# Kernel tuning notes

Hardware: AMD Instinct MI355X
Metric: run time of the kernel (lower is better)

## Reference

```python
import jax, jax.numpy as jnp
import numpy as np

DIM = 64; PDIM = 16; HEADS = 8; WS = 10; KS = 13; NBLK = 2
B = 4; H = 200; W = 200


def conv2d(x, w, b=None, padding=0, groups=1):
    out = jax.lax.conv_general_dilated(
        x, w, (1, 1), [(padding, padding), (padding, padding)],
        dimension_numbers=('NCHW', 'OIHW', 'NCHW'), feature_group_count=groups)
    if b is not None:
        out = out + b[None, :, None, None]
    return out


def gelu(x):
    return jax.nn.gelu(x, approximate=False)  # torch default exact gelu


def layernorm_cf(x, w, b, eps=1e-6):
    # channels_first LayerNorm: normalize over channel axis (axis=1)
    mu = jnp.mean(x, axis=1, keepdims=True)
    var = jnp.mean((x - mu) ** 2, axis=1, keepdims=True)
    return (x - mu) * jax.lax.rsqrt(var + eps) * w[None, :, None, None] + b[None, :, None, None]


def conv_ffn(x, pw, pb, dw, db, aw, ab):
    x = gelu(conv2d(x, pw, pb))
    x = gelu(conv2d(x, dw, db, padding=dw.shape[-1] // 2, groups=x.shape[1])) + x
    return conv2d(x, aw, ab)


def geo_ensemble(k):
    k = jax.lax.stop_gradient(k)  # torch code uses .detach()
    kr = jnp.rot90(k, k=-1, axes=(2, 3))
    s = k + k[:, :, :, ::-1] + k[:, :, ::-1, :] + k[:, :, ::-1, ::-1]
    s = s + kr + kr[:, :, :, ::-1] + kr[:, :, ::-1, :] + kr[:, :, ::-1, ::-1]
    return s / 8.0


def rpe_bias(rpb, ws):
    idx = jnp.arange(ws * ws)
    h_, w_ = idx // ws, idx % ws
    rel_h = h_[None, :] - h_[:, None] + ws - 1  # k_h - q_h
    rel_w = w_[None, :] - w_[:, None] + ws - 1
    rel_idx = rel_h * (2 * ws - 1) + rel_w
    return rpb[:, rel_idx]  # [heads, N, N]


def window_attention(x, qw, qb, ow, ob, rpb):
    b, c, h, w = x.shape  # h, w divisible by WS
    hd, wd = h // WS, w // WS
    ch = c // HEADS
    qkv = conv2d(x, qw, qb)  # [b, 3c, h, w]
    t = qkv.reshape(b, 3, HEADS, ch, hd, WS, wd, WS)
    t = t.transpose(1, 0, 4, 6, 2, 5, 7, 3).reshape(3, b * hd * wd, HEADS, WS * WS, ch)
    q, k, v = t[0], t[1], t[2]
    bias = rpe_bias(rpb, WS)[None]  # [1, heads, N, N]
    score = jnp.einsum('whqc,whkc->whqk', q, k) / jnp.sqrt(jnp.float32(ch)) + bias
    attn = jax.nn.softmax(score, axis=-1)
    out = jnp.einsum('whqk,whkc->whqc', attn, v)
    out = out.reshape(b, hd, wd, HEADS, WS, WS, ch).transpose(0, 3, 6, 1, 4, 2, 5).reshape(b, c, h, w)
    return conv2d(out, ow, ob)


def conv_attention(x, lk, d1w, d1b, d2w, d2b):
    bs, c, h, w = x.shape
    x1, x2 = x[:, :PDIM], x[:, PDIM:]
    g = jnp.mean(x1, axis=(2, 3), keepdims=True)  # AdaptiveAvgPool2d(1)
    g = gelu(conv2d(g, d1w, d1b))
    dk = conv2d(g, d2w, d2b).reshape(bs * PDIM, 1, 3, 3)  # per-sample dw kernels
    x1d = conv2d(x1.reshape(1, bs * PDIM, h, w), dk, padding=1, groups=bs * PDIM)
    x1d = x1d.reshape(bs, PDIM, h, w)
    x1 = conv2d(x1, lk, padding=KS // 2) + x1d
    return jnp.concatenate([x1, x2], axis=1)


def _forward(x, ln_proj_w, ln_proj_b, proj_p_w, proj_p_b, proj_d_w, proj_d_b, proj_a_w, proj_a_b,
             ln_attn_w, ln_attn_b, qkv_w, qkv_b, attn_out_w, attn_out_b, rpb,
             dwcp1_w, dwcp1_b, dwcp2_w, dwcp2_b, pconv_aggr_w, pconv_aggr_b,
             ffn_p_w, ffn_p_b, ffn_d_w, ffn_d_b, ffn_a_w, ffn_a_b,
             ln_out_w, ln_out_b, conv_out_w, conv_out_b, plk_filter):
    skip = x
    x = layernorm_cf(x, ln_proj_w, ln_proj_b)
    x = conv_ffn(x, proj_p_w, proj_p_b, proj_d_w, proj_d_b, proj_a_w, proj_a_b)
    x = x + window_attention(layernorm_cf(x, ln_attn_w, ln_attn_b), qkv_w, qkv_b, attn_out_w, attn_out_b, rpb)
    lk = geo_ensemble(plk_filter)
    for i in range(NBLK):  # lns are Identity (use_ln=False)
        y = conv_ffn(x, ffn_p_w[i], ffn_p_b[i], ffn_d_w[i], ffn_d_b[i], ffn_a_w[i], ffn_a_b[i])
        y = conv_attention(y, lk, dwcp1_w[i], dwcp1_b[i], dwcp2_w[i], dwcp2_b[i])
        y = conv2d(y, pconv_aggr_w[i], pconv_aggr_b[i])
        x = x + y
    x = conv2d(layernorm_cf(x, ln_out_w, ln_out_b), conv_out_w, conv_out_b, padding=1)
    return x + skip


def setup_inputs() -> dict:
    key = jax.random.key(0)
    ks = jax.random.split(key, 20)
    def rn(i, shape, scale):
        return jax.random.normal(ks[i], shape, dtype=jnp.float32) * scale
    inp = {
        'x': rn(0, (B, DIM, H, W), 1.0),
        'ln_proj_w': jnp.ones(DIM, jnp.float32), 'ln_proj_b': jnp.zeros(DIM, jnp.float32),
        'proj_p_w': rn(1, (128, 64, 1, 1), 64 ** -0.5), 'proj_p_b': jnp.zeros(128, jnp.float32),
        'proj_d_w': rn(2, (128, 1, 3, 3), 1.0 / 3.0), 'proj_d_b': jnp.zeros(128, jnp.float32),
        'proj_a_w': rn(3, (64, 128, 1, 1), 128 ** -0.5), 'proj_a_b': jnp.zeros(64, jnp.float32),
        'ln_attn_w': jnp.ones(DIM, jnp.float32), 'ln_attn_b': jnp.zeros(DIM, jnp.float32),
        'qkv_w': rn(4, (192, 64, 1, 1), 64 ** -0.5), 'qkv_b': jnp.zeros(192, jnp.float32),
        'attn_out_w': rn(5, (64, 64, 1, 1), 64 ** -0.5), 'attn_out_b': jnp.zeros(64, jnp.float32),
        'rpb': rn(6, (HEADS, (2 * WS - 1) ** 2), 0.001),
        'dwcp1_w': rn(7, (2, 8, 16, 1, 1), 16 ** -0.5), 'dwcp1_b': jnp.zeros((2, 8), jnp.float32),
        'dwcp2_w': rn(8, (2, 144, 8, 1, 1), 0.01), 'dwcp2_b': jnp.zeros((2, 144), jnp.float32),
        'pconv_aggr_w': rn(9, (2, 64, 64, 1, 1), 64 ** -0.5), 'pconv_aggr_b': jnp.zeros((2, 64), jnp.float32),
        'ffn_p_w': rn(10, (2, 80, 64, 1, 1), 64 ** -0.5), 'ffn_p_b': jnp.zeros((2, 80), jnp.float32),
        'ffn_d_w': rn(11, (2, 80, 1, 3, 3), 1.0 / 3.0), 'ffn_d_b': jnp.zeros((2, 80), jnp.float32),
        'ffn_a_w': rn(12, (2, 64, 80, 1, 1), 80 ** -0.5), 'ffn_a_b': jnp.zeros((2, 64), jnp.float32),
        'ln_out_w': jnp.ones(DIM, jnp.float32), 'ln_out_b': jnp.zeros(DIM, jnp.float32),
        'conv_out_w': rn(13, (64, 64, 3, 3), (64 * 9) ** -0.5), 'conv_out_b': jnp.zeros(64, jnp.float32),
        'plk_filter': rn(14, (PDIM, PDIM, KS, KS), (PDIM * KS * KS) ** -0.5),
    }
    return inp


def reference(x, ln_proj_w, ln_proj_b, proj_p_w, proj_p_b, proj_d_w, proj_d_b, proj_a_w, proj_a_b,
              ln_attn_w, ln_attn_b, qkv_w, qkv_b, attn_out_w, attn_out_b, rpb,
              dwcp1_w, dwcp1_b, dwcp2_w, dwcp2_b, pconv_aggr_w, pconv_aggr_b,
              ffn_p_w, ffn_p_b, ffn_d_w, ffn_d_b, ffn_a_w, ffn_a_b,
              ln_out_w, ln_out_b, conv_out_w, conv_out_b, plk_filter):
    return _forward(x, ln_proj_w, ln_proj_b, proj_p_w, proj_p_b, proj_d_w, proj_d_b, proj_a_w, proj_a_b,
                    ln_attn_w, ln_attn_b, qkv_w, qkv_b, attn_out_w, attn_out_b, rpb,
                    dwcp1_w, dwcp1_b, dwcp2_w, dwcp2_b, pconv_aggr_w, pconv_aggr_b,
                    ffn_p_w, ffn_p_b, ffn_d_w, ffn_d_b, ffn_a_w, ffn_a_b,
                    ln_out_w, ln_out_b, conv_out_w, conv_out_b, plk_filter)
```

## Files before the change

kernel.cpp:

```cpp
#include <hip/hip_runtime.h>
#include <math.h>

#define HH 200
#define WW 200
#define HWP 40000
#define NP4 10000
#define BB 4

#define LKS 40
#define DPS 24
#define PARTSZ 2560000

typedef __fp16 f16x2 __attribute__((ext_vector_type(2)));
typedef __fp16 f16x8 __attribute__((ext_vector_type(8)));
typedef float fx4 __attribute__((ext_vector_type(4)));

#if __has_builtin(__builtin_amdgcn_fdot2)
__device__ __forceinline__ float fdot2f(f16x2 a, f16x2 b, float c) {
    return __builtin_amdgcn_fdot2(a, b, c, false);
}
#else
__device__ __forceinline__ float fdot2f(f16x2 a, f16x2 b, float c) {
    return c + (float)a[0] * (float)b[0] + (float)a[1] * (float)b[1];
}
#endif

__device__ __forceinline__ f16x2 pk2(float a, float b) {
    return __builtin_amdgcn_cvt_pkrtz(a, b);
}

__device__ __forceinline__ float gelu_f(float x) {
    return 0.5f * x * (1.0f + erff(x * 0.7071067811865475f));
}

__global__ __launch_bounds__(256) void prep_kernel(
    const float* __restrict__ pc, f16x2* __restrict__ wth)
{
    int i = blockIdx.x * 256 + threadIdx.x;
    if (i >= 4096) return;
    int w = i >> 11;
    int r = i & 2047;
    int c2 = r / 64, o = r - c2 * 64;
    const float* src = pc + w * 4096;
    f16x2 v;
    v[0] = (__fp16)src[o * 64 + 2 * c2];
    v[1] = (__fp16)src[o * 64 + 2 * c2 + 1];
    wth[w * 2048 + r] = v;
}

__global__ __launch_bounds__(256) void prepA_kernel(
    const float* __restrict__ qkvw, const float* __restrict__ pp,
    const float* __restrict__ ao, const float* __restrict__ fp,
    f16x8* __restrict__ wA)
{
    int s = blockIdx.x * 256 + threadIdx.x;
    if (s >= 4352) return;
    const float* src;
    int base;
    if (s < 1536)      { src = qkvw;      base = 0; }
    else if (s < 2560) { src = pp;        base = 1536; }
    else if (s < 3072) { src = ao;        base = 2560; }
    else if (s < 3712) { src = fp;        base = 3072; }
    else               { src = fp + 5120; base = 3712; }
    int r = s - base;
    int lane = r & 63;
    int t = r >> 6;
    int ks = t & 1;
    int cot = t >> 1;
    int co = cot * 16 + (lane & 15);
    int k0 = ks * 32 + ((lane >> 4) << 3);
    f16x8 v;
#pragma unroll
    for (int j = 0; j < 8; ++j) v[j] = (__fp16)src[co * 64 + k0 + j];
    wA[s] = v;
}

__global__ __launch_bounds__(256) void prepA2_kernel(
    const float* __restrict__ pa, const float* __restrict__ fa,
    f16x8* __restrict__ wA2)
{
    int s = blockIdx.x * 256 + threadIdx.x;
    if (s >= 2560) return;
    const float* src; int base, Ci, ksteps;
    if (s < 1024)      { src = pa;        base = 0;    Ci = 128; ksteps = 4; }
    else if (s < 1792) { src = fa;        base = 1024; Ci = 80;  ksteps = 3; }
    else               { src = fa + 5120; base = 1792; Ci = 80;  ksteps = 3; }
    int r = s - base;
    int lane = r & 63;
    int u = r >> 6;
    int ks = u % ksteps;
    int cot = u / ksteps;
    int co = cot * 16 + (lane & 15);
    int k0 = ks * 32 + ((lane >> 4) << 3);
    f16x8 v;
#pragma unroll
    for (int j = 0; j < 8; ++j) {
        int k = k0 + j;
        v[j] = (k < Ci) ? (__fp16)src[co * Ci + k] : (__fp16)0.f;
    }
    wA2[s] = v;
}

__global__ __launch_bounds__(256) void prepA3_kernel(
    const float* __restrict__ co3, f16x8* __restrict__ wA3)
{
    int s = blockIdx.x * 256 + threadIdx.x;
    if (s >= 4608) return;
    int lane = s & 63;
    int u = s >> 6;
    int cot = u & 3;
    int t = u >> 2;
    int co = cot * 16 + (lane & 15);
    int k0 = t * 32 + ((lane >> 4) << 3);
    f16x8 v;
#pragma unroll
    for (int j = 0; j < 8; ++j) {
        int k = k0 + j;
        int tap = k >> 6, ci = k & 63;
        v[j] = (__fp16)co3[(co * 64 + ci) * 9 + tap];
    }
    wA3[s] = v;
}

__global__ __launch_bounds__(256, 2) void ln_kernel(
    const float* __restrict__ in, const float* __restrict__ w,
    const float* __restrict__ b, __fp16* __restrict__ out)
{
    int p = blockIdx.x * 256 + threadIdx.x;
    int bb = blockIdx.y;
    if (p >= HWP) return;
    const float* ib = in + (size_t)bb * 64 * HWP + p;
    float v[64];
    float mu = 0.f;
#pragma unroll
    for (int c = 0; c < 64; ++c) { v[c] = ib[(size_t)c * HWP]; mu += v[c]; }
    mu *= (1.f / 64.f);
    float var = 0.f;
#pragma unroll
    for (int c = 0; c < 64; ++c) { float d = v[c] - mu; var += d * d; }
    var *= (1.f / 64.f);
    float r = rsqrtf(var + 1e-6f);
    __fp16* ob = out + (size_t)bb * 64 * HWP + p;
#pragma unroll
    for (int c = 0; c < 64; ++c) ob[(size_t)c * HWP] = (__fp16)((v[c] - mu) * r * w[c] + b[c]);
}

__global__ __launch_bounds__(256, 2) void lnconvh_kernel(
    const float* __restrict__ in,
    const float* __restrict__ lnw, const float* __restrict__ lnb,
    const f16x8* __restrict__ wA,
    const float* __restrict__ bias, __fp16* __restrict__ outh,
    int Co, int do_gelu)
{
    int lane = threadIdx.x & 63;
    int wv = threadIdx.x >> 6;
    int px0 = blockIdx.x * 256 + wv * 64;
    if (px0 >= HWP) return;
    int bb = blockIdx.z;
    int cot0 = blockIdx.y * 4;
    int nCot = (Co >> 4) - cot0; if (nCot > 4) nCot = 4;
    int row = lane >> 4;
    int colp = lane & 15;

    float wl[2][8], bl[2][8];
#pragma unroll
    for (int ks = 0; ks < 2; ++ks)
#pragma unroll
        for (int j = 0; j < 8; ++j) {
            int c = ks * 32 + row * 8 + j;
            wl[ks][j] = lnw[c];
            bl[ks][j] = lnb[c];
        }

    f16x8 afr[4][2];
#pragma unroll
    for (int c = 0; c < 4; ++c)
        if (c < nCot)
#pragma unroll
            for (int ks = 0; ks < 2; ++ks)
                afr[c][ks] = wA[(((cot0 + c) * 2 + ks) << 6) + lane];

    fx4 acc[4][4];
#pragma unroll
    for (int c = 0; c < 4; ++c)
#pragma unroll
        for (int nt = 0; nt < 4; ++nt)
#pragma unroll
            for (int r = 0; r < 4; ++r) acc[c][nt][r] = 0.f;

    const float* ib = in + (size_t)bb * 64 * HWP;
#pragma unroll
    for (int nt = 0; nt < 4; ++nt) {
        int px = px0 + nt * 16 + colp;
        float xv[2][8];
        float s = 0.f, sq = 0.f;
#pragma unroll
        for (int ks = 0; ks < 2; ++ks)
#pragma unroll
            for (int j = 0; j < 8; ++j) {
                float v = ib[(size_t)(ks * 32 + row * 8 + j) * HWP + px];
                xv[ks][j] = v;
                s += v; sq += v * v;
            }
        s += __shfl_xor(s, 16, 64);  sq += __shfl_xor(sq, 16, 64);
        s += __shfl_xor(s, 32, 64);  sq += __shfl_xor(sq, 32, 64);
        float mu = s * (1.f / 64.f);
        float var = sq * (1.f / 64.f) - mu * mu;
        float rr = rsqrtf(fmaxf(var, 0.f) + 1e-6f);
#pragma unroll
        for (int ks = 0; ks < 2; ++ks) {
            union { f16x8 v; f16x2 h[4]; } bu;
#pragma unroll
            for (int j2 = 0; j2 < 4; ++j2) {
                float v0 = (xv[ks][2 * j2]     - mu) * rr * wl[ks][2 * j2]     + bl[ks][2 * j2];
                float v1 = (xv[ks][2 * j2 + 1] - mu) * rr * wl[ks][2 * j2 + 1] + bl[ks][2 * j2 + 1];
                bu.h[j2] = pk2(v0, v1);
            }
#pragma unroll
            for (int c = 0; c < 4; ++c)
                if (c < nCot)
                    acc[c][nt] = __builtin_amdgcn_mfma_f32_16x16x32_f16(afr[c][ks], bu.v, acc[c][nt], 0, 0, 0);
        }
    }

#pragma unroll
    for (int c = 0; c < 4; ++c) {
        if (c < nCot) {
#pragma unroll
            for (int r = 0; r < 4; ++r) {
                int co = (cot0 + c) * 16 + row * 4 + r;
                float bv = bias[co];
#pragma unroll
                for (int nt = 0; nt < 4; ++nt) {
                    int px = px0 + nt * 16 + colp;
                    float v = acc[c][nt][r] + bv;
                    if (do_gelu) v = gelu_f(v);
                    outh[((size_t)bb * Co + co) * HWP + px] = (__fp16)v;
                }
            }
        }
    }
}

__global__ __launch_bounds__(256, 2) void conv1x1_mfma_kernel(
    const float* __restrict__ in, const f16x8* __restrict__ wA,
    const float* __restrict__ bias, float* outf, __fp16* outh,
    int Co, int do_gelu, int do_add)
{
    int lane = threadIdx.x & 63;
    int wv = threadIdx.x >> 6;
    int px0 = blockIdx.x * 256 + wv * 64;
    if (px0 >= HWP) return;
    int bb = blockIdx.z;
    int cot0 = blockIdx.y * 4;
    int nCot = (Co >> 4) - cot0; if (nCot > 4) nCot = 4;
    int row = lane >> 4;
    int colp = lane & 15;

    fx4 acc[4][4];
#pragma unroll
    for (int c = 0; c < 4; ++c)
#pragma unroll
        for (int nt = 0; nt < 4; ++nt)
#pragma unroll
            for (int r = 0; r < 4; ++r) acc[c][nt][r] = 0.f;

    const float* ib = in + (size_t)bb * 64 * HWP;
#pragma unroll
    for (int ks = 0; ks < 2; ++ks) {
        f16x8 afr[4];
#pragma unroll
        for (int c = 0; c < 4; ++c)
            if (c < nCot) afr[c] = wA[(((cot0 + c) * 2 + ks) << 6) + lane];
#pragma unroll
        for (int nt = 0; nt < 4; ++nt) {
            int px = px0 + nt * 16 + colp;
            const float* bp = ib + (size_t)(ks * 32 + row * 8) * HWP + px;
            union { f16x8 v; f16x2 h[4]; } bu;
            bu.h[0] = pk2(bp[0],              bp[(size_t)1 * HWP]);
            bu.h[1] = pk2(bp[(size_t)2 * HWP], bp[(size_t)3 * HWP]);
            bu.h[2] = pk2(bp[(size_t)4 * HWP], bp[(size_t)5 * HWP]);
            bu.h[3] = pk2(bp[(size_t)6 * HWP], bp[(size_t)7 * HWP]);
#pragma unroll
            for (int c = 0; c < 4; ++c)
                if (c < nCot)
                    acc[c][nt] = __builtin_amdgcn_mfma_f32_16x16x32_f16(afr[c], bu.v, acc[c][nt], 0, 0, 0);
        }
    }

#pragma unroll
    for (int c = 0; c < 4; ++c) {
        if (c < nCot) {
#pragma unroll
            for (int r = 0; r < 4; ++r) {
                int co = (cot0 + c) * 16 + row * 4 + r;
                float bv = bias[co];
#pragma unroll
                for (int nt = 0; nt < 4; ++nt) {
                    int px = px0 + nt * 16 + colp;
                    float v = acc[c][nt][r] + bv;
                    if (do_gelu) v = gelu_f(v);
                    if (outh) {
                        outh[((size_t)bb * Co + co) * HWP + px] = (__fp16)v;
                    } else {
                        float* op = outf + ((size_t)bb * Co + co) * HWP;
                        if (do_add) v += op[px];
                        op[px] = v;
                    }
                }
            }
        }
    }
}

__global__ __launch_bounds__(256, 2) void convh_kernel(
    const __fp16* __restrict__ in,
    const f16x8* __restrict__ wA,
    const float* __restrict__ bias, float* outf, __fp16* outh,
    int Ci, int ksteps, int Co, int do_gelu, int do_add)
{
    int lane = threadIdx.x & 63;
    int wv = threadIdx.x >> 6;
    int px0 = blockIdx.x * 256 + wv * 64;
    if (px0 >= HWP) return;
    int bb = blockIdx.z;
    int cot0 = blockIdx.y * 4;
    int nCot = (Co >> 4) - cot0; if (nCot > 4) nCot = 4;
    int row = lane >> 4;
    int colp = lane & 15;

    fx4 acc[4][4];
#pragma unroll
    for (int c = 0; c < 4; ++c)
#pragma unroll
        for (int nt = 0; nt < 4; ++nt)
#pragma unroll
            for (int r = 0; r < 4; ++r) acc[c][nt][r] = 0.f;

    const __fp16* ib = in + (size_t)bb * Ci * HWP;
    for (int ks = 0; ks < ksteps; ++ks) {
        f16x8 afr[4];
#pragma unroll
        for (int c = 0; c < 4; ++c)
            if (c < nCot) afr[c] = wA[(((cot0 + c) * ksteps + ks) << 6) + lane];
        int k0 = ks * 32 + row * 8;
        bool ok = (k0 < Ci);
#pragma unroll
        for (int nt = 0; nt < 4; ++nt) {
            int px = px0 + nt * 16 + colp;
            f16x8 bv;
            if (ok) {
                const __fp16* bp = ib + (size_t)k0 * HWP + px;
#pragma unroll
                for (int j = 0; j < 8; ++j) bv[j] = bp[(size_t)j * HWP];
            } else {
#pragma unroll
                for (int j = 0; j < 8; ++j) bv[j] = (__fp16)0.f;
            }
#pragma unroll
            for (int c = 0; c < 4; ++c)
                if (c < nCot)
                    acc[c][nt] = __builtin_amdgcn_mfma_f32_16x16x32_f16(afr[c], bv, acc[c][nt], 0, 0, 0);
        }
    }

#pragma unroll
    for (int c = 0; c < 4; ++c) {
        if (c < nCot) {
#pragma unroll
            for (int r = 0; r < 4; ++r) {
                int co = (cot0 + c) * 16 + row * 4 + r;
                float bv = bias[co];
#pragma unroll
                for (int nt = 0; nt < 4; ++nt) {
                    int px = px0 + nt * 16 + colp;
                    float v = acc[c][nt][r] + bv;
                    if (do_gelu) v = gelu_f(v);
                    if (outh) {
                        outh[((size_t)bb * Co + co) * HWP + px] = (__fp16)v;
                    } else {
                        float* op = outf + ((size_t)bb * Co + co) * HWP;
                        if (do_add) v += op[px];
                        op[px] = v;
                    }
                }
            }
        }
    }
}

__global__ __launch_bounds__(256, 2) void conv3_mfma_kernel(
    const __fp16* __restrict__ in,
    const f16x8* __restrict__ wA3,
    const float* __restrict__ bias, const float* __restrict__ skip,
    float* __restrict__ out)
{
    int lane = threadIdx.x & 63;
    int wv = threadIdx.x >> 6;
    int px0 = blockIdx.x * 256 + wv * 64;
    if (px0 >= HWP) return;
    int bb = blockIdx.z;
    int row = lane >> 4;
    int colp = lane & 15;

    fx4 acc[4][4];
#pragma unroll
    for (int c = 0; c < 4; ++c)
#pragma unroll
        for (int nt = 0; nt < 4; ++nt)
#pragma unroll
            for (int r = 0; r < 4; ++r) acc[c][nt][r] = 0.f;

    int py[4], pxx[4];
#pragma unroll
    for (int nt = 0; nt < 4; ++nt) {
        int p = px0 + nt * 16 + colp;
        py[nt] = p / WW;
        pxx[nt] = p - py[nt] * WW;
    }

    const __fp16* ib = in + (size_t)bb * 64 * HWP;
    for (int t = 0; t < 18; ++t) {
        int tap = t >> 1, ks = t & 1;
        int dy = tap / 3 - 1, dx = tap % 3 - 1;
        f16x8 afr[4];
#pragma unroll
        for (int c = 0; c < 4; ++c) afr[c] = wA3[((t * 4 + c) << 6) + lane];
        const __fp16* kb = ib + (size_t)(ks * 32 + row * 8) * HWP;
#pragma unroll
        for (int nt = 0; nt < 4; ++nt) {
            int yy = py[nt] + dy, xx = pxx[nt] + dx;
            f16x8 bv;
            if ((unsigned)yy < HH && (unsigned)xx < WW) {
                const __fp16* bp = kb + yy * WW + xx;
#pragma unroll
                for (int j = 0; j < 8; ++j) bv[j] = bp[(size_t)j * HWP];
            } else {
#pragma unroll
                for (int j = 0; j < 8; ++j) bv[j] = (__fp16)0.f;
            }
#pragma unroll
            for (int c = 0; c < 4; ++c)
                acc[c][nt] = __builtin_amdgcn_mfma_f32_16x16x32_f16(afr[c], bv, acc[c][nt], 0, 0, 0);
        }
    }

#pragma unroll
    for (int c = 0; c < 4; ++c) {
#pragma unroll
        for (int r = 0; r < 4; ++r) {
            int co = c * 16 + row * 4 + r;
            float bv = bias[co];
            const float* sb = skip + ((size_t)bb * 64 + co) * HWP;
            float* op = out + ((size_t)bb * 64 + co) * HWP;
#pragma unroll
            for (int nt = 0; nt < 4; ++nt) {
                int px = px0 + nt * 16 + colp;
                op[px] = acc[c][nt][r] + bv + sb[px];
            }
        }
    }
}

__global__ __launch_bounds__(256, 4) void dwgelu_kernel(
    const __fp16* __restrict__ in,
    const float* __restrict__ dw,
    const float* __restrict__ db,
    __fp16* __restrict__ vout,
    int Ci)
{
    __shared__ float s_p[16][18 * DPS];
    int tid = threadIdx.x;
    int tx = tid & 15, ty = tid >> 4;
    int x0 = blockIdx.x * 16, y0 = blockIdx.y * 16;
    int part = blockIdx.z & 3;
    int bb = blockIdx.z >> 2;
    int cic = Ci >> 2;
    int cbase = part * cic;
    int x = x0 + tx, y = y0 + ty;
    bool inb = (x < WW && y < HH);
    int p = y * WW + x;

    const __fp16* ibase = in + (size_t)bb * Ci * HWP;
    __fp16* obase = vout + (size_t)bb * Ci * HWP;
    for (int c0 = cbase; c0 < cbase + cic; c0 += 16) {
        int chunk = cbase + cic - c0; if (chunk > 16) chunk = 16;
        __syncthreads();
        for (int i = tid; i < chunk * 324; i += 256) {
            int ci = i / 324; int r = i - ci * 324;
            int py = r / 18, px = r - py * 18;
            int yy = y0 + py - 1, xx = x0 + px - 1;
            float v = 0.f;
            if ((unsigned)yy < HH && (unsigned)xx < WW)
                v = (float)ibase[(size_t)(c0 + ci) * HWP + yy * WW + xx];
            s_p[ci][py * DPS + px] = v;
        }
        __syncthreads();
        if (inb) {
            for (int ci = 0; ci < chunk; ++ci) {
                int c = c0 + ci;
                float s = db[c];
                const float* dwr = dw + c * 9;
#pragma unroll
                for (int ky = 0; ky < 3; ++ky)
#pragma unroll
                    for (int kx = 0; kx < 3; ++kx)
                        s += s_p[ci][(ty + ky) * DPS + tx + kx] * dwr[ky * 3 + kx];
                float v = gelu_f(s) + s_p[ci][(ty + 1) * DPS + tx + 1];
                obase[(size_t)c * HWP + p] = (__fp16)v;
            }
        }
    }
}

__global__ __launch_bounds__(128, 4) void winattn2_kernel(
    const __fp16* __restrict__ qkv,
    const float* __restrict__ rpb,
    __fp16* __restrict__ out)
{
    __shared__ __align__(16) f16x2 s_k2[100][4];
    __shared__ __align__(4) __fp16 s_vT[8][100];
    __shared__ float s_b[361];

    int lin = blockIdx.x + 400 * (blockIdx.y + 8 * blockIdx.z);
    int swz = (lin & 7) * 1600 + (lin >> 3);
    int win = swz % 400;
    int head = (swz / 400) & 7;
    int bb = swz / 3200;
    int wy = win / 20, wx = win - wy * 20;
    int tid = threadIdx.x;

    const float log2e = 1.4426950408889634f;
    for (int i = tid; i < 361; i += 128) s_b[i] = rpb[head * 361 + i] * log2e;

    int ty = tid / 10, tx = tid - ty * 10;
    f16x2 q2[4];
    if (tid < 100) {
        int y = wy * 10 + ty, x = wx * 10 + tx;
        int gp = y * WW + x;
        const __fp16* qb = qkv + ((size_t)bb * 192 + head * 8) * HWP + gp;
        const __fp16* kb = qb + (size_t)64 * HWP;
        const __fp16* vb = qb + (size_t)128 * HWP;
        const float qsc = 0.3535533905932738f * log2e;
#pragma unroll
        for (int c2 = 0; c2 < 4; ++c2) {
            q2[c2] = pk2((float)qb[(size_t)(2 * c2) * HWP] * qsc,
                         (float)qb[(size_t)(2 * c2 + 1) * HWP] * qsc);
            f16x2 kv;
            kv[0] = kb[(size_t)(2 * c2) * HWP];
            kv[1] = kb[(size_t)(2 * c2 + 1) * HWP];
            s_k2[tid][c2] = kv;
        }
#pragma unroll
        for (int cc = 0; cc < 8; ++cc)
            s_vT[cc][tid] = vb[(size_t)cc * HWP];
    }
    __syncthreads();

    if (tid < 100) {
        const float* brow = s_b + (180 - ty * 19 - tx);

        f16x2 s16[50];
        float m = -1e30f;
#pragma unroll
        for (int i = 0; i < 50; ++i) {
            const int k0 = 2 * i, k1 = 2 * i + 1;
            const int c0 = (k0 / 10) * 19 + (k0 % 10);
            const int c1 = (k1 / 10) * 19 + (k1 % 10);
            float s0 = brow[c0];
            float s1 = brow[c1];
#pragma unroll
            for (int c2 = 0; c2 < 4; ++c2) {
                s0 = fdot2f(q2[c2], s_k2[k0][c2], s0);
                s1 = fdot2f(q2[c2], s_k2[k1][c2], s1);
            }
            m = fmaxf(m, fmaxf(s0, s1));
            s16[i] = pk2(s0, s1);
        }
        float l = 0.f;
        float o[8];
#pragma unroll
        for (int cc = 0; cc < 8; ++cc) o[cc] = 0.f;
#pragma unroll
        for (int i = 0; i < 50; ++i) {
            float e0 = exp2f((float)s16[i][0] - m);
            float e1 = exp2f((float)s16[i][1] - m);
            l += e0 + e1;
            f16x2 e2 = pk2(e0, e1);
#pragma unroll
            for (int cc = 0; cc < 8; ++cc)
                o[cc] = fdot2f(e2, *(const f16x2*)&s_vT[cc][2 * i], o[cc]);
        }
        float rl = 1.f / l;
        int y = wy * 10 + ty, x = wx * 10 + tx;
        __fp16* ob = out + ((size_t)bb * 64 + head * 8) * HWP + y * WW + x;
#pragma unroll
        for (int cc = 0; cc < 8; ++cc) ob[(size_t)cc * HWP] = (__fp16)(o[cc] * rl);
    }
}

__global__ __launch_bounds__(256) void geo_kernel(
    const float* __restrict__ k, f16x2* __restrict__ out)
{
    int i = blockIdx.x * 256 + threadIdx.x;
    if (i >= 3584) return;
    int p = i / 448;
    int r = i - p * 448;
    int rep = r >> 4, co = r & 15;
    int a = 0, rr = rep;
    while (rr >= 7 - a) { rr -= 7 - a; ++a; }
    int b2 = a + rr;
    int y = 6 + a, x = 6 + b2;
    float sv[2];
#pragma unroll
    for (int t = 0; t < 2; ++t) {
        int ci = 2 * p + t;
        const float* kb = k + (co * 16 + ci) * 169;
        float s = kb[y * 13 + x] + kb[y * 13 + (12 - x)] + kb[(12 - y) * 13 + x] + kb[(12 - y) * 13 + (12 - x)]
                + kb[(12 - x) * 13 + y] + kb[x * 13 + y] + kb[(12 - x) * 13 + (12 - y)] + kb[x * 13 + (12 - y)];
        sv[t] = s * 0.125f;
    }
    f16x2 v;
    v[0] = (__fp16)sv[0];
    v[1] = (__fp16)sv[1];
    out[i] = v;
}

__global__ __launch_bounds__(256) void gmean_kernel(
    const float* __restrict__ in, float* __restrict__ g)
{
    int bc = blockIdx.x;
    int bb = bc >> 4, c = bc & 15;
    const float* p = in + ((size_t)bb * 64 + c) * HWP;
    float s = 0.f;
    for (int i = threadIdx.x; i < HWP; i += 256) s += p[i];
#pragma unroll
    for (int off = 32; off > 0; off >>= 1) s += __shfl_down(s, off);
    __shared__ float red[4];
    int wave = threadIdx.x >> 6;
    if ((threadIdx.x & 63) == 0) red[wave] = s;
    __syncthreads();
    if (threadIdx.x == 0)
        g[bc] = (red[0] + red[1] + red[2] + red[3]) * (1.f / 40000.f);
}

__global__ __launch_bounds__(192) void dynk_kernel(
    const float* __restrict__ g, const float* __restrict__ w1, const float* __restrict__ b1,
    const float* __restrict__ w2, const float* __restrict__ b2, float* __restrict__ dk)
{
    int bb = blockIdx.x;
    __shared__ float s_g2[8];
    int tid = threadIdx.x;
    if (tid < 8) {
        float a = b1[tid];
        for (int c = 0; c < 16; ++c) a += w1[tid * 16 + c] * g[bb * 16 + c];
        s_g2[tid] = gelu_f(a);
    }
    __syncthreads();
    if (tid < 144) {
        float a = b2[tid];
#pragma unroll
        for (int i = 0; i < 8; ++i) a += w2[tid * 8 + i] * s_g2[i];
        dk[bb * 144 + tid] = a;
    }
}

__global__ __launch_bounds__(256, 6) void lkconv_kernel(
    const float* __restrict__ in,
    const f16x2* __restrict__ lkP,
    const float* __restrict__ dk,
    float* __restrict__ out)
{
    __shared__ f16x2 s_p[2][28 * LKS];
    int z = blockIdx.z;
    int bb = z >> 2, q = z & 3;
    int tid = threadIdx.x;
    int tx = tid & 15, ty = tid >> 4;
    int x0 = blockIdx.x * 16, y0 = blockIdx.y * 16;
    int x = x0 + tx, y = y0 + ty;

    const float* ib = in + ((size_t)bb * 64 + q * 4) * HWP;
    for (int i = tid; i < 2 * 784; i += 256) {
        int pi = i / 784; int r = i - pi * 784;
        int py = r / 28, px = r - py * 28;
        int yy = y0 + py - 6, xx = x0 + px - 6;
        f16x2 v = pk2(0.f, 0.f);
        if ((unsigned)yy < HH && (unsigned)xx < WW) {
            int gp = yy * WW + xx;
            v = pk2(ib[(size_t)(2 * pi) * HWP + gp], ib[(size_t)(2 * pi + 1) * HWP + gp]);
        }
        s_p[pi][py * LKS + px] = v;
    }
    __syncthreads();

    float acc[16];
#pragma unroll
    for (int co = 0; co < 16; ++co) acc[co] = 0.f;

#pragma unroll
    for (int pi = 0; pi < 2; ++pi) {
        f16x2 orb[28];
#pragma unroll
        for (int o = 0; o < 28; ++o) orb[o] = pk2(0.f, 0.f);
#pragma unroll
        for (int ky = 0; ky < 13; ++ky) {
#pragma unroll
            for (int kx = 0; kx < 13; ++kx) {
                const int a = (ky < 6) ? (6 - ky) : (ky - 6);
                const int b = (kx < 6) ? (6 - kx) : (kx - 6);
                const int lo = (a < b) ? a : b;
                const int hi = (a < b) ? b : a;
                const int idx = lo * 7 - (lo * (lo - 1)) / 2 + (hi - lo);
                orb[idx] += s_p[pi][(ty + ky) * LKS + tx + kx];
            }
        }
        const f16x2* wci = lkP + (size_t)(q * 2 + pi) * 28 * 16;
#pragma unroll
        for (int o = 0; o < 28; ++o) {
            f16x2 ov = orb[o];
            const f16x2* wr = wci + o * 16;
#pragma unroll
            for (int co = 0; co < 16; ++co) acc[co] = fdot2f(ov, wr[co], acc[co]);
        }
#pragma unroll
        for (int h = 0; h < 2; ++h) {
            int ci = q * 4 + 2 * pi + h;
            float d = 0.f;
            const float* dkr = dk + bb * 144 + ci * 9;
#pragma unroll
            for (int dy = 0; dy < 3; ++dy)
#pragma unroll
                for (int dx = 0; dx < 3; ++dx)
                    d += (float)s_p[pi][(ty + 5 + dy) * LKS + tx + 5 + dx][h] * dkr[dy * 3 + dx];
#pragma unroll
            for (int co = 0; co < 16; ++co) acc[co] += (co == ci) ? d : 0.f;
        }
    }

    if (x < WW && y < HH) {
        int p = y * WW + x;
        float* ob = out + (size_t)q * PARTSZ + (size_t)bb * 16 * HWP + p;
#pragma unroll
        for (int co = 0; co < 16; ++co) ob[(size_t)co * HWP] = acc[co];
    }
}

__global__ __launch_bounds__(256, 2) void pconv_add_kernel(
    const float* __restrict__ x1q,
    const float* __restrict__ yy,
    const f16x2* __restrict__ wt,
    const float* __restrict__ bias,
    float* __restrict__ xout)
{
    int p4 = blockIdx.x * 256 + threadIdx.x;
    int o0 = blockIdx.y * 16;
    int bb = blockIdx.z;
    if (p4 >= NP4) return;
    float4 acc[16];
#pragma unroll
    for (int j = 0; j < 16; ++j) {
        float bv = bias[o0 + j];
        acc[j] = make_float4(bv, bv, bv, bv);
    }
    const float4* xb0 = (const float4*)(x1q + (size_t)bb * 16 * HWP) + p4;
    const float4* xb1 = (const float4*)(x1q + PARTSZ + (size_t)bb * 16 * HWP) + p4;
    const float4* xb2 = (const float4*)(x1q + 2 * PARTSZ + (size_t)bb * 16 * HWP) + p4;
    const float4* xb3 = (const float4*)(x1q + 3 * PARTSZ + (size_t)bb * 16 * HWP) + p4;
    for (int c2 = 0; c2 < 8; ++c2) {
        int ca = 2 * c2, cb = 2 * c2 + 1;
        float4 a0 = xb0[(size_t)ca * NP4], a1 = xb1[(size_t)ca * NP4];
        float4 a2 = xb2[(size_t)ca * NP4], a3 = xb3[(size_t)ca * NP4];
        float4 s0;
        s0.x = (a0.x + a1.x) + (a2.x + a3.x);
        s0.y = (a0.y + a1.y) + (a2.y + a3.y);
        s0.z = (a0.z + a1.z) + (a2.z + a3.z);
        s0.w = (a0.w + a1.w) + (a2.w + a3.w);
        a0 = xb0[(size_t)cb * NP4]; a1 = xb1[(size_t)cb * NP4];
        a2 = xb2[(size_t)cb * NP4]; a3 = xb3[(size_t)cb * NP4];
        float4 s1;
        s1.x = (a0.x + a1.x) + (a2.x + a3.x);
        s1.y = (a0.y + a1.y) + (a2.y + a3.y);
        s1.z = (a0.z + a1.z) + (a2.z + a3.z);
        s1.w = (a0.w + a1.w) + (a2.w + a3.w);
        f16x2 px = pk2(s0.x, s1.x), py = pk2(s0.y, s1.y);
        f16x2 pz = pk2(s0.z, s1.z), pw = pk2(s0.w, s1.w);
        const f16x2* wr = wt + c2 * 64 + o0;
#pragma unroll
        for (int j = 0; j < 16; ++j) {
            f16x2 w = wr[j];
            acc[j].x = fdot2f(px, w, acc[j].x);
            acc[j].y = fdot2f(py, w, acc[j].y);
            acc[j].z = fdot2f(pz, w, acc[j].z);
            acc[j].w = fdot2f(pw, w, acc[j].w);
        }
    }
    const float4* yb = (const float4*)(yy + ((size_t)bb * 64 + 16) * HWP) + p4;
    for (int c2 = 8; c2 < 32; ++c2) {
        int cy = 2 * (c2 - 8);
        float4 s0 = yb[(size_t)cy * NP4];
        float4 s1 = yb[(size_t)(cy + 1) * NP4];
        f16x2 px = pk2(s0.x, s1.x), py = pk2(s0.y, s1.y);
        f16x2 pz = pk2(s0.z, s1.z), pw = pk2(s0.w, s1.w);
        const f16x2* wr = wt + c2 * 64 + o0;
#pragma unroll
        for (int j = 0; j < 16; ++j) {
            f16x2 w = wr[j];
            acc[j].x = fdot2f(px, w, acc[j].x);
            acc[j].y = fdot2f(py, w, acc[j].y);
            acc[j].z = fdot2f(pz, w, acc[j].z);
            acc[j].w = fdot2f(pw, w, acc[j].w);
        }
    }
    float4* ob = (float4*)(xout + ((size_t)bb * 64 + o0) * HWP) + p4;
#pragma unroll
    for (int j = 0; j < 16; ++j) {
        float4 old = ob[(size_t)j * NP4];
        old.x += acc[j].x; old.y += acc[j].y; old.z += acc[j].z; old.w += acc[j].w;
        ob[(size_t)j * NP4] = old;
    }
}

extern "C" void kernel_launch(void* const* d_in, const int* in_sizes, int n_in,
                              void* d_out, int out_size, void* d_ws, size_t ws_size,
                              hipStream_t stream)
{
    const float* x_in      = (const float*)d_in[0];
    const float* ln_proj_w = (const float*)d_in[1];
    const float* ln_proj_b = (const float*)d_in[2];
    const float* proj_p_w  = (const float*)d_in[3];
    const float* proj_p_b  = (const float*)d_in[4];
    const float* proj_d_w  = (const float*)d_in[5];
    const float* proj_d_b  = (const float*)d_in[6];
    const float* proj_a_w  = (const float*)d_in[7];
    const float* proj_a_b  = (const float*)d_in[8];
    const float* ln_attn_w = (const float*)d_in[9];
    const float* ln_attn_b = (const float*)d_in[10];
    const float* qkv_w     = (const float*)d_in[11];
    const float* qkv_b     = (const float*)d_in[12];
    const float* attn_o_w  = (const float*)d_in[13];
    const float* attn_o_b  = (const float*)d_in[14];
    const float* rpb       = (const float*)d_in[15];
    const float* dwcp1_w   = (const float*)d_in[16];
    const float* dwcp1_b   = (const float*)d_in[17];
    const float* dwcp2_w   = (const float*)d_in[18];
    const float* dwcp2_b   = (const float*)d_in[19];
    const float* pconv_w   = (const float*)d_in[20];
    const float* pconv_b   = (const float*)d_in[21];
    const float* ffn_p_w   = (const float*)d_in[22];
    const float* ffn_p_b   = (const float*)d_in[23];
    const float* ffn_d_w   = (const float*)d_in[24];
    const float* ffn_d_b   = (const float*)d_in[25];
    const float* ffn_a_w   = (const float*)d_in[26];
    const float* ffn_a_b   = (const float*)d_in[27];
    const float* ln_out_w  = (const float*)d_in[28];
    const float* ln_out_b  = (const float*)d_in[29];
    const float* conv_o_w  = (const float*)d_in[30];
    const float* conv_o_b  = (const float*)d_in[31];
    const float* plk       = (const float*)d_in[32];

    float* X  = (float*)d_out;
    float* ws = (float*)d_ws;

    float*  Y    = ws;
    __fp16* A16  = (__fp16*)ws;
    __fp16* R1h  = (__fp16*)(ws + 10240000);
    __fp16* QKVh = (__fp16*)(ws + 10240000);
    __fp16* Vh   = (__fp16*)(ws + 23040000);
    float*  R2Q  = ws + 33280000;
    f16x2* LKTH = (f16x2*)(ws + 43520000);
    float* GM   = ws + 43524096;
    float* DK   = GM + 64;
    f16x2* WTH  = (f16x2*)(DK + 576);
    f16x8* WAH  = (f16x8*)(DK + 576 + 4096);
    f16x8* WA2  = WAH + 4352;
    f16x8* WA3  = WA2 + 2560;

    dim3 b256(256);
    dim3 gLN(157, 4);
    dim3 gT16(13, 13, 16);

    prep_kernel<<<dim3(16), b256, 0, stream>>>(pconv_w, WTH);
    prepA_kernel<<<dim3(17), b256, 0, stream>>>(qkv_w, proj_p_w, attn_o_w, ffn_p_w, WAH);
    prepA2_kernel<<<dim3(10), b256, 0, stream>>>(proj_a_w, ffn_a_w, WA2);
    prepA3_kernel<<<dim3(18), b256, 0, stream>>>(conv_o_w, WA3);
    geo_kernel<<<dim3(14), b256, 0, stream>>>(plk, LKTH);

    lnconvh_kernel<<<dim3(157, 2, 4), b256, 0, stream>>>(x_in, ln_proj_w, ln_proj_b,
                                                         WAH + 1536, proj_p_b, R1h, 128, 1);
    dwgelu_kernel<<<gT16, b256, 0, stream>>>(R1h, proj_d_w, proj_d_b, Vh, 128);
    convh_kernel<<<dim3(157, 1, 4), b256, 0, stream>>>(Vh, WA2 + 0, proj_a_b,
                                                       X, nullptr, 128, 4, 64, 0, 0);

    lnconvh_kernel<<<dim3(157, 3, 4), b256, 0, stream>>>(X, ln_attn_w, ln_attn_b,
                                                         WAH + 0, qkv_b, QKVh, 192, 0);
    winattn2_kernel<<<dim3(400, 8, 4), dim3(128), 0, stream>>>(QKVh, rpb, A16);
    convh_kernel<<<dim3(157, 1, 4), b256, 0, stream>>>(A16, WAH + 2560, attn_o_b,
                                                       X, nullptr, 64, 2, 64, 0, 1);

    for (int i = 0; i < 2; ++i) {
        conv1x1_mfma_kernel<<<dim3(157, 2, 4), b256, 0, stream>>>(X, WAH + 3072 + i * 640,
                                                                  ffn_p_b + i * 80, nullptr, R1h, 80, 1, 0);
        dwgelu_kernel<<<gT16, b256, 0, stream>>>(R1h, ffn_d_w + i * 720, ffn_d_b + i * 80, Vh, 80);
        convh_kernel<<<dim3(157, 1, 4), b256, 0, stream>>>(Vh, WA2 + 1024 + i * 768,
                                                           ffn_a_b + i * 64, Y, nullptr, 80, 3, 64, 0, 0);
        gmean_kernel<<<dim3(64), b256, 0, stream>>>(Y, GM);
        dynk_kernel<<<dim3(4), dim3(192), 0, stream>>>(GM, dwcp1_w + i * 128, dwcp1_b + i * 8,
                                                       dwcp2_w + i * 1152, dwcp2_b + i * 144, DK);
        lkconv_kernel<<<gT16, b256, 0, stream>>>(Y, LKTH, DK, R2Q);
        pconv_add_kernel<<<dim3(40, 4, 4), b256, 0, stream>>>(R2Q, Y, WTH + i * 2048, pconv_b + i * 64, X);
    }

    ln_kernel<<<gLN, b256, 0, stream>>>(X, ln_out_w, ln_out_b, A16);
    conv3_mfma_kernel<<<dim3(157, 1, 4), b256, 0, stream>>>(A16, WA3, conv_o_b, x_in, X);
}
```

Before: 923.1 us.

## Rewrite window attention to use MFMA 16x16x32 for QK and PV

Replaces the per-thread fdot2 window attention with a two-wave MFMA formulation. K and V fragments sit in registers, scores come from 16x16x32 f16 MFMAs over 7 key tiles, and the softmax probabilities are staged in LDS for a second MFMA against V. This is meant to cut the scalar ALU cost of the attention. In exchange it pads 100 tokens up to 112, wastes half the K dimension, since only 8 of the 32 channels are real, and raises register and LDS use, with launch bounds lowered from 4 to 3.

Measured after the change: 970.4 us. 5.1% more time.

```diff
diff --git a/kernel.cpp b/kernel.cpp
--- a/kernel.cpp
+++ b/kernel.cpp
@@ -513,13 +513,12 @@
     }
 }
 
-__global__ __launch_bounds__(128, 4) void winattn2_kernel(
+__global__ __launch_bounds__(128, 3) void winattn3_kernel(
     const __fp16* __restrict__ qkv,
     const float* __restrict__ rpb,
     __fp16* __restrict__ out)
 {
-    __shared__ __align__(16) f16x2 s_k2[100][4];
-    __shared__ __align__(4) __fp16 s_vT[8][100];
+    __shared__ __align__(16) __fp16 s_ph[112 * 136];
     __shared__ float s_b[361];
 
     int lin = blockIdx.x + 400 * (blockIdx.y + 8 * blockIdx.z);
@@ -529,73 +528,142 @@
     int bb = swz / 3200;
     int wy = win / 20, wx = win - wy * 20;
     int tid = threadIdx.x;
+    int wave = tid >> 6, lane = tid & 63;
+    int colp = lane & 15, rg = lane >> 4;
 
     const float log2e = 1.4426950408889634f;
+    const float qsc = 0.3535533905932738f * log2e;
+
+    const __fp16* qb = qkv + ((size_t)bb * 192 + head * 8) * HWP;
+    const __fp16* kb = qb + (size_t)64 * HWP;
+    const __fp16* vb = qb + (size_t)128 * HWP;
+
     for (int i = tid; i < 361; i += 128) s_b[i] = rpb[head * 361 + i] * log2e;
-
-    int ty = tid / 10, tx = tid - ty * 10;
-    f16x2 q2[4];
-    if (tid < 100) {
-        int y = wy * 10 + ty, x = wx * 10 + tx;
-        int gp = y * WW + x;
-        const __fp16* qb = qkv + ((size_t)bb * 192 + head * 8) * HWP + gp;
-        const __fp16* kb = qb + (size_t)64 * HWP;
-        const __fp16* vb = qb + (size_t)128 * HWP;
-        const float qsc = 0.3535533905932738f * log2e;
-#pragma unroll
-        for (int c2 = 0; c2 < 4; ++c2) {
-            q2[c2] = pk2((float)qb[(size_t)(2 * c2) * HWP] * qsc,
-                         (float)qb[(size_t)(2 * c2 + 1) * HWP] * qsc);
-            f16x2 kv;
-            kv[0] = kb[(size_t)(2 * c2) * HWP];
-            kv[1] = kb[(size_t)(2 * c2 + 1) * HWP];
-            s_k2[tid][c2] = kv;
-        }
-#pragma unroll
-        for (int cc = 0; cc < 8; ++cc)
-            s_vT[cc][tid] = vb[(size_t)cc * HWP];
-    }
+    for (int i = tid; i < 112 * 8; i += 128) {
+        int qr = i >> 3, sl = i & 7;
+        *(f16x2*)&s_ph[qr * 136 + 112 + 2 * sl] = pk2(0.f, 0.f);
+    }
+
+    f16x8 kfr[7];
+#pragma unroll
+    for (int mt = 0; mt < 7; ++mt) {
+        f16x8 v;
+        int key = mt * 16 + colp;
+        if (rg == 0 && key < 100) {
+            int gp = (wy * 10 + key / 10) * WW + wx * 10 + key % 10;
+#pragma unroll
+            for (int j = 0; j < 8; ++j) v[j] = kb[(size_t)j * HWP + gp];
+        } else {
+#pragma unroll
+            for (int j = 0; j < 8; ++j) v[j] = (__fp16)0.f;
+        }
+        kfr[mt] = v;
+    }
+    f16x8 vfr[4];
+#pragma unroll
+    for (int ks = 0; ks < 4; ++ks) {
+        f16x8 v;
+#pragma unroll
+        for (int j = 0; j < 8; ++j) {
+            int key = ks * 32 + rg * 8 + j;
+            __fp16 val = (__fp16)0.f;
+            if (colp < 8 && key < 100) {
+                int gp = (wy * 10 + key / 10) * WW + wx * 10 + key % 10;
+                val = vb[(size_t)colp * HWP + gp];
+            }
+            v[j] = val;
+        }
+        vfr[ks] = v;
+    }
+    int bidx[7][4];
+#pragma unroll
+    for (int mt = 0; mt < 7; ++mt)
+#pragma unroll
+        for (int r = 0; r < 4; ++r) {
+            int key = mt * 16 + rg * 4 + r;
+            int kk = key < 100 ? key : 0;
+            bidx[mt][r] = (kk / 10) * 19 + (kk % 10);
+        }
+
     __syncthreads();
 
-    if (tid < 100) {
-        const float* brow = s_b + (180 - ty * 19 - tx);
-
-        f16x2 s16[50];
-        float m = -1e30f;
-#pragma unroll
-        for (int i = 0; i < 50; ++i) {
-            const int k0 = 2 * i, k1 = 2 * i + 1;
-            const int c0 = (k0 / 10) * 19 + (k0 % 10);
-            const int c1 = (k1 / 10) * 19 + (k1 % 10);
-            float s0 = brow[c0];
-            float s1 = brow[c1];
-#pragma unroll
-            for (int c2 = 0; c2 < 4; ++c2) {
-                s0 = fdot2f(q2[c2], s_k2[k0][c2], s0);
-                s1 = fdot2f(q2[c2], s_k2[k1][c2], s1);
-            }
-            m = fmaxf(m, fmaxf(s0, s1));
-            s16[i] = pk2(s0, s1);
-        }
-        float l = 0.f;
-        float o[8];
-#pragma unroll
-        for (int cc = 0; cc < 8; ++cc) o[cc] = 0.f;
-#pragma unroll
-        for (int i = 0; i < 50; ++i) {
-            float e0 = exp2f((float)s16[i][0] - m);
-            float e1 = exp2f((float)s16[i][1] - m);
-            l += e0 + e1;
-            f16x2 e2 = pk2(e0, e1);
-#pragma unroll
-            for (int cc = 0; cc < 8; ++cc)
-                o[cc] = fdot2f(e2, *(const f16x2*)&s_vT[cc][2 * i], o[cc]);
-        }
-        float rl = 1.f / l;
-        int y = wy * 10 + ty, x = wx * 10 + tx;
-        __fp16* ob = out + ((size_t)bb * 64 + head * 8) * HWP + y * WW + x;
-#pragma unroll
-        for (int cc = 0; cc < 8; ++cc) ob[(size_t)cc * HWP] = (__fp16)(o[cc] * rl);
+    int ntBeg = wave ? 4 : 0;
+    int ntEnd = wave ? 7 : 4;
+    float rlv[4];
+
+#pragma unroll
+    for (int t = 0; t < 4; ++t) {
+        int nt = ntBeg + t;
+        if (nt < ntEnd) {
+            int q = nt * 16 + colp;
+            f16x8 qf;
+            if (rg == 0 && q < 100) {
+                int gp = (wy * 10 + q / 10) * WW + wx * 10 + q % 10;
+#pragma unroll
+                for (int j = 0; j < 8; ++j) qf[j] = (__fp16)((float)qb[(size_t)j * HWP + gp] * qsc);
+            } else {
+#pragma unroll
+                for (int j = 0; j < 8; ++j) qf[j] = (__fp16)0.f;
+            }
+            fx4 sc[7];
+#pragma unroll
+            for (int mt = 0; mt < 7; ++mt)
+                sc[mt] = __builtin_amdgcn_mfma_f32_16x16x32_f16(kfr[mt], qf, (fx4){0.f, 0.f, 0.f, 0.f}, 0, 0, 0);
+            int qq = q < 100 ? q : 0;
+            int boff = 180 - (qq / 10) * 19 - (qq % 10);
+            float m = -1e30f;
+#pragma unroll
+            for (int mt = 0; mt < 7; ++mt) {
+#pragma unroll
+                for (int r = 0; r < 4; ++r) {
+                    int key = mt * 16 + rg * 4 + r;
+                    float s = (key < 100) ? (sc[mt][r] + s_b[bidx[mt][r] + boff]) : -1e30f;
+                    sc[mt][r] = s;
+                    m = fmaxf(m, s);
+                }
+            }
+            m = fmaxf(m, __shfl_xor(m, 16, 64));
+            m = fmaxf(m, __shfl_xor(m, 32, 64));
+            float l = 0.f;
+#pragma unroll
+            for (int mt = 0; mt < 7; ++mt) {
+                float e0 = exp2f(sc[mt][0] - m);
+                float e1 = exp2f(sc[mt][1] - m);
+                float e2 = exp2f(sc[mt][2] - m);
+                float e3 = exp2f(sc[mt][3] - m);
+                l += (e0 + e1) + (e2 + e3);
+                f16x2* dst = (f16x2*)&s_ph[q * 136 + mt * 16 + rg * 4];
+                dst[0] = pk2(e0, e1);
+                dst[1] = pk2(e2, e3);
+            }
+            l += __shfl_xor(l, 16, 64);
+            l += __shfl_xor(l, 32, 64);
+            rlv[t] = 1.f / l;
+        }
+    }
+
+#pragma unroll
+    for (int t = 0; t < 4; ++t) {
+        int nt = ntBeg + t;
+        if (nt < ntEnd) {
+            fx4 o = {0.f, 0.f, 0.f, 0.f};
+#pragma unroll
+            for (int ks = 0; ks < 4; ++ks) {
+                f16x8 pf = *(const f16x8*)&s_ph[(nt * 16 + colp) * 136 + ks * 32 + rg * 8];
+                o = __builtin_amdgcn_mfma_f32_16x16x32_f16(vfr[ks], pf, o, 0, 0, 0);
+            }
+            int q = nt * 16 + colp;
+            if (q < 100) {
+                int gp = (wy * 10 + q / 10) * WW + wx * 10 + q % 10;
+                float rr = rlv[t];
+#pragma unroll
+                for (int r = 0; r < 4; ++r) {
+                    int ch = rg * 4 + r;
+                    if (ch < 8)
+                        out[((size_t)bb * 64 + head * 8 + ch) * HWP + gp] = (__fp16)(o[r] * rr);
+                }
+            }
+        }
     }
 }
 
@@ -893,7 +961,7 @@
 
     lnconvh_kernel<<<dim3(157, 3, 4), b256, 0, stream>>>(X, ln_attn_w, ln_attn_b,
                                                          WAH + 0, qkv_b, QKVh, 192, 0);
-    winattn2_kernel<<<dim3(400, 8, 4), dim3(128), 0, stream>>>(QKVh, rpb, A16);
+    winattn3_kernel<<<dim3(400, 8, 4), dim3(128), 0, stream>>>(QKVh, rpb, A16);
     convh_kernel<<<dim3(157, 1, 4), b256, 0, stream>>>(A16, WAH + 2560, attn_o_b,
                                                        X, nullptr, 64, 2, 64, 0, 1);
 
```
